# Optimization experiments

Measured on AMD Instinct MI355X. Metric: run time of the kernel, lower is better.

Reference implementation:

```python
import jax, jax.numpy as jnp
import numpy as np
from jax import lax

SOS_TOKEN = 0
PAD_LEN = 30  # tokenizer.pad_len -> number of greedy decode steps


def _gru_cell(x, h, w_ih, w_hh, b_ih, b_hh):
    # PyTorch GRU cell math. x,h: [B,H]; w_*: [3H,H]; b_*: [3H]
    gi = x @ w_ih.T + b_ih
    gh = h @ w_hh.T + b_hh
    i_r, i_z, i_n = jnp.split(gi, 3, axis=-1)
    h_r, h_z, h_n = jnp.split(gh, 3, axis=-1)
    r = jax.nn.sigmoid(i_r + h_r)
    z = jax.nn.sigmoid(i_z + h_z)
    n = jnp.tanh(i_n + r * h_n)
    return (1.0 - z) * n + z * h


def _sm_encode(sm_hidden, conv_w, conv_b, enc_w, enc_b):
    # sm_hidden: [B, L, C] -> conv over time with C input channels
    x = jnp.transpose(sm_hidden, (0, 2, 1))  # [B, C, L]
    conv = lax.conv_general_dilated(
        x, conv_w, window_strides=(1,), padding='VALID',
        dimension_numbers=('NCH', 'OIH', 'NCH'))  # [B, O, L-k+1]
    conv = jax.nn.relu(conv + conv_b[None, :, None])
    pooled = jnp.max(conv, axis=-1)  # [B, O]
    return jax.nn.relu(pooled @ enc_w.T + enc_b)  # [B, H]


def reference(sm_hidden, embedding, w_ih, w_hh, b_ih, b_hh,
              w_out, b_out, conv_w, conv_b, enc_w, enc_b):
    B = sm_hidden.shape[0]
    h0 = _sm_encode(sm_hidden, conv_w, conv_b, enc_w, enc_b)  # [B, H]

    # The original re-runs the GRU over the whole (append-only) prefix each
    # iteration; since the GRU is deterministic this equals incremental
    # single-step updates, which we do here.
    def step(carry, _):
        h, tok = carry
        emb = embedding[tok]                      # [B, H]
        h_new = _gru_cell(emb, h, w_ih, w_hh, b_ih, b_hh)
        logits = h_new @ w_out.T + b_out          # [B, V]
        tok_new = jnp.argmax(logits, axis=-1)     # greedy topk(1)
        return (h_new, tok_new), (h_new, tok_new)

    tok0 = jnp.full((B,), SOS_TOKEN, dtype=jnp.int32)
    (h_last, _), (hiddens, toks) = lax.scan(step, (h0, tok0), None, length=PAD_LEN)

    decoder_output = jax.nn.log_softmax(h_last @ w_out.T + b_out, axis=1)  # [B, V]
    decoder_hidden = hiddens  # [PAD_LEN, B, H] == rnn_out of final _base_forward
    decoded_indices = jnp.concatenate([tok0[None, :], toks], axis=0)  # [PAD_LEN+1, B]
    return decoder_output, decoder_hidden, decoded_indices


def setup_inputs() -> dict:
    key = jax.random.key(0)
    ks = jax.random.split(key, 12)
    B, L, C = 512, 120, 128
    H, V, O, K = 1024, 512, 32, 10
    s = 1.0 / np.sqrt(H)
    return {
        'sm_hidden': jax.random.normal(ks[0], (B, L, C), jnp.float32),
        'embedding': jax.random.normal(ks[1], (V, H), jnp.float32),
        'w_ih': jax.random.uniform(ks[2], (3 * H, H), jnp.float32, -s, s),
        'w_hh': jax.random.uniform(ks[3], (3 * H, H), jnp.float32, -s, s),
        'b_ih': jax.random.uniform(ks[4], (3 * H,), jnp.float32, -s, s),
        'b_hh': jax.random.uniform(ks[5], (3 * H,), jnp.float32, -s, s),
        'w_out': jax.random.uniform(ks[6], (V, H), jnp.float32, -s, s),
        'b_out': jax.random.uniform(ks[7], (V,), jnp.float32, -s, s),
        'conv_w': jax.random.normal(ks[8], (O, C, K), jnp.float32) * 0.05,
        'conv_b': jax.random.normal(ks[9], (O,), jnp.float32) * 0.05,
        'enc_w': jax.random.uniform(ks[10], (H, O), jnp.float32, -s, s),
        'enc_b': jax.random.uniform(ks[11], (H,), jnp.float32, -s, s),
    }
```

## Files before the change

### kernel.cpp

```cpp
#include <hip/hip_runtime.h>
#include <hip/hip_bf16.h>
#include <math.h>

#define Bsz 512
#define Hd 1024
#define Vd 512
#define Cc 128
#define Ll 120
#define Kk 10
#define Oo 32
#define NSTEP 30

typedef __attribute__((ext_vector_type(8))) short bf16x8;
typedef __attribute__((ext_vector_type(4))) float f32x4;
typedef unsigned short ushort;
typedef unsigned long long u64;

static __device__ __forceinline__ float sigm(float x) { return 1.f / (1.f + expf(-x)); }
static __device__ __forceinline__ ushort f2bf(float x) {
    __hip_bfloat16 h = __float2bfloat16(x);
    return *(ushort*)&h;
}
static __device__ __forceinline__ float bf2f(ushort u) {
    __hip_bfloat16 h; *(ushort*)&h = u;
    return __bfloat162float(h);
}
static __device__ __forceinline__ unsigned monofy(float f) {
    unsigned u = __float_as_uint(f);
    return (u & 0x80000000u) ? ~u : (u | 0x80000000u);
}

__global__ void k_split(const float* __restrict__ in, ushort* __restrict__ hi,
                        ushort* __restrict__ lo, int n) {
    int i = blockIdx.x * 256 + threadIdx.x;
    if (i < n) {
        float v = in[i];
        ushort h = f2bf(v);
        hi[i] = h;
        lo[i] = f2bf(v - bf2f(h));
    }
}

__global__ void k_pack(const float* __restrict__ W, ushort* __restrict__ hi,
                       ushort* __restrict__ lo, int total) {
    int idx = blockIdx.x * 256 + threadIdx.x;
    if (idx >= total) return;
    int jj = idx & 7, l = (idx >> 3) & 63, c = (idx >> 9) & 31, nf = idx >> 14;
    int n = nf * 16 + (l & 15);
    int k = c * 32 + ((l >> 4) << 3) + jj;
    float v = W[(size_t)n * 1024 + k];
    ushort h = f2bf(v);
    hi[idx] = h;
    lo[idx] = f2bf(v - bf2f(h));
}

__global__ void k_packconv(const float* __restrict__ cw, ushort* __restrict__ hi,
                           ushort* __restrict__ lo) {
    int idx = blockIdx.x * 256 + threadIdx.x;
    if (idx >= 2 * 40 * 64 * 8) return;
    int jj = idx & 7, l = (idx >> 3) & 63, ch = (idx >> 9) % 40, nf = idx / (40 * 512);
    int o = nf * 16 + (l & 15);
    int k = ch * 32 + ((l >> 4) << 3) + jj;
    int kc = k >> 7, c = k & 127;
    float v = cw[(o * Cc + c) * Kk + kc];
    ushort h = f2bf(v);
    hi[idx] = h;
    lo[idx] = f2bf(v - bf2f(h));
}

__global__ __launch_bounds__(256) void k_convmfma(const ushort* __restrict__ xH,
                                                  const ushort* __restrict__ xL,
                                                  const ushort* __restrict__ wH,
                                                  const ushort* __restrict__ wL,
                                                  const float* __restrict__ cb,
                                                  const float* __restrict__ ew,
                                                  const float* __restrict__ eb,
                                                  float* __restrict__ h0,
                                                  ushort* __restrict__ ApHi,
                                                  ushort* __restrict__ ApLo) {
    __shared__ float sred[4][2][16];
    __shared__ float ps[Oo];
    int tid = threadIdx.x, wid = tid >> 6, l = tid & 63;

    for (int b2 = 0; b2 < 2; ++b2) {
        int b = blockIdx.x * 2 + b2;
        f32x4 acc[2][2];
#pragma unroll
        for (int i = 0; i < 2; ++i)
#pragma unroll
            for (int j = 0; j < 2; ++j) acc[i][j] = (f32x4)0.f;

        bf16x8 aH0[2], aL0[2], bH0[2], bL0[2];
        bf16x8 aH1[2], aL1[2], bH1[2], bL1[2];

#define CLD(AH, AL, BH, BL, ch)                                                        \
    {                                                                                  \
        _Pragma("unroll") for (int tf2 = 0; tf2 < 2; ++tf2) {                          \
            int aoff = ((b * 120 + (wid * 2 + tf2) * 16 + (l & 15) + ((ch) >> 2)) * 128 \
                        + ((ch) & 3) * 32 + ((l >> 4) << 3));                          \
            AH[tf2] = *(const bf16x8*)(xH + aoff);                                     \
            AL[tf2] = *(const bf16x8*)(xL + aoff);                                     \
        }                                                                              \
        _Pragma("unroll") for (int nf = 0; nf < 2; ++nf) {                             \
            int boff = ((nf * 40 + (ch)) * 64 + l) * 8;                                \
            BH[nf] = *(const bf16x8*)(wH + boff);                                      \
            BL[nf] = *(const bf16x8*)(wL + boff);                                      \
        }                                                                              \
    }
#define CST(AH, AL, BH, BL)                                                            \
    {                                                                                  \
        _Pragma("unroll") for (int tf2 = 0; tf2 < 2; ++tf2)                            \
            _Pragma("unroll") for (int nf = 0; nf < 2; ++nf) {                         \
                acc[tf2][nf] = __builtin_amdgcn_mfma_f32_16x16x32_bf16(                \
                    AH[tf2], BH[nf], acc[tf2][nf], 0, 0, 0);                           \
                acc[tf2][nf] = __builtin_amdgcn_mfma_f32_16x16x32_bf16(                \
                    AH[tf2], BL[nf], acc[tf2][nf], 0, 0, 0);                           \
                acc[tf2][nf] = __builtin_amdgcn_mfma_f32_16x16x32_bf16(                \
                    AL[tf2], BH[nf], acc[tf2][nf], 0, 0, 0);                           \
            }                                                                          \
    }

        CLD(aH0, aL0, bH0, bL0, 0)
#pragma unroll
        for (int ch = 0; ch < 40; ch += 2) {
            CLD(aH1, aL1, bH1, bL1, ch + 1)
            CST(aH0, aL0, bH0, bL0)
            if (ch + 2 < 40) CLD(aH0, aL0, bH0, bL0, ch + 2)
            CST(aH1, aL1, bH1, bL1)
        }
#undef CLD
#undef CST

        float mx[2] = {-1e38f, -1e38f};
#pragma unroll
        for (int tf2 = 0; tf2 < 2; ++tf2) {
            int tb = (wid * 2 + tf2) * 16 + ((l >> 4) << 2);
#pragma unroll
            for (int q = 0; q < 4; ++q) {
                if (tb + q <= 110) {
                    mx[0] = fmaxf(mx[0], acc[tf2][0][q]);
                    mx[1] = fmaxf(mx[1], acc[tf2][1][q]);
                }
            }
        }
#pragma unroll
        for (int s = 16; s < 64; s <<= 1) {
            mx[0] = fmaxf(mx[0], __shfl_xor(mx[0], s));
            mx[1] = fmaxf(mx[1], __shfl_xor(mx[1], s));
        }
        if (l < 16) {
            sred[wid][0][l] = mx[0];
            sred[wid][1][l] = mx[1];
        }
        __syncthreads();
        if (tid < Oo) {
            float m = sred[0][tid >> 4][tid & 15];
#pragma unroll
            for (int w = 1; w < 4; ++w) m = fmaxf(m, sred[w][tid >> 4][tid & 15]);
            ps[tid] = fmaxf(m + cb[tid], 0.f);
        }
        __syncthreads();
        for (int j = tid; j < Hd; j += 256) {
            float a = eb[j];
            const float4* e4 = (const float4*)(ew + (size_t)j * Oo);
#pragma unroll
            for (int c4 = 0; c4 < 8; ++c4) {
                float4 w = e4[c4];
                a += ps[c4 * 4 + 0] * w.x + ps[c4 * 4 + 1] * w.y +
                     ps[c4 * 4 + 2] * w.z + ps[c4 * 4 + 3] * w.w;
            }
            a = fmaxf(a, 0.f);
            h0[(size_t)b * Hd + j] = a;
            ushort hb = f2bf(a);
            ushort lb = f2bf(a - bf2f(hb));
            int c = j >> 5, sub = (j >> 3) & 3, jj = j & 7, mf = b >> 4;
            int lane_r = (b & 15) + (sub << 4);
            int flat = ((mf * 32 + c) * 64 + lane_r) * 8 + jj;
            ApHi[flat] = hb;
            ApLo[flat] = lb;
        }
        __syncthreads();
    }
}

template <int EPI>
__global__ __launch_bounds__(512, 4) void k_rnn(const ushort* __restrict__ Ah,
                                                const ushort* __restrict__ Al,
                                                const ushort* __restrict__ Bh,
                                                const ushort* __restrict__ Bl,
                                                const float* __restrict__ bias,
                                                float* __restrict__ outF,
                                                const float* __restrict__ gi_all,
                                                const u64* __restrict__ pkRd,
                                                u64* __restrict__ pkWr,
                                                float* __restrict__ outIdxRow,
                                                const float* __restrict__ hOld,
                                                ushort* __restrict__ ApHi,
                                                ushort* __restrict__ ApLo) {
    __shared__ ushort Bs[2][24][512];
    int id = blockIdx.x;
    int xcd = id & 7, r = id >> 3;
    int jt = xcd * 4 + (r & 3);
    int mt = r >> 2;
    int tid = threadIdx.x, wid = tid >> 6, l = tid & 63;
    int wm = wid >> 1, wj = wid & 1;
    int mf = mt * 4 + wm;
    int jf = jt * 2 + wj;
    int jcol = jf * 16 + (l & 15);

    float giR[4][3], hR[4];
    int bR[4], tkR[4];
    if constexpr (EPI == 1) {
#pragma unroll
        for (int q = 0; q < 4; ++q) {
            bR[q] = mf * 16 + ((l >> 4) << 2) + q;
            u64 pk = pkRd[bR[q]];
            tkR[q] = 511 - (int)(unsigned)(pk & 0xFFFFFFFFu);
            const float* gi = gi_all + (size_t)tkR[q] * 3072;
            giR[q][0] = gi[jcol];
            giR[q][1] = gi[1024 + jcol];
            giR[q][2] = gi[2048 + jcol];
            hR[q] = hOld[(size_t)bR[q] * 1024 + jcol];
        }
        if (jt == 0 && wj == 0 && (l & 15) == 0) {
#pragma unroll
            for (int q = 0; q < 4; ++q) {
                pkWr[bR[q]] = 0ULL;
                if (outIdxRow) outIdxRow[bR[q]] = (float)tkR[q];
            }
        }
    }

    f32x4 acc[3];
#pragma unroll
    for (int g = 0; g < 3; ++g) acc[g] = (f32x4)0.f;

    bf16x8 stg[3], aH0[2], aL0[2], aH1[2], aL1[2];

#define STG_LD(it)                                                                     \
    {                                                                                  \
        _Pragma("unroll") for (int k = 0; k < 3; ++k) {                                \
            int u = wid + 8 * k;                                                       \
            int hl = u & 1, wjb = (u >> 1) & 1, g = (u >> 2) % 3, cu = u / 12;         \
            const ushort* sp = hl ? Bl : Bh;                                           \
            stg[k] = *(const bf16x8*)(sp +                                             \
                (size_t)(((g * 64 + jt * 2 + wjb) * 32 + (it) * 2 + cu) * 64 + l) * 8);\
        }                                                                              \
    }
#define STG_WR(buf)                                                                    \
    {                                                                                  \
        _Pragma("unroll") for (int k = 0; k < 3; ++k)                                  \
            *(bf16x8*)&Bs[buf][wid + 8 * k][l * 8] = stg[k];                           \
    }
#define A_LD(DH, DL, it)                                                               \
    {                                                                                  \
        _Pragma("unroll") for (int cc = 0; cc < 2; ++cc) {                             \
            DH[cc] = *(const bf16x8*)(Ah + (size_t)((mf * 32 + (it) * 2 + cc) * 64 + l) * 8); \
            DL[cc] = *(const bf16x8*)(Al + (size_t)((mf * 32 + (it) * 2 + cc) * 64 + l) * 8); \
        }                                                                              \
    }
#define CMP(buf, AH, AL)                                                               \
    {                                                                                  \
        _Pragma("unroll") for (int cc = 0; cc < 2; ++cc)                               \
            _Pragma("unroll") for (int g = 0; g < 3; ++g) {                            \
                bf16x8 bhh = *(const bf16x8*)&Bs[buf][cc * 12 + g * 4 + wj * 2 + 0][l * 8]; \
                bf16x8 bll = *(const bf16x8*)&Bs[buf][cc * 12 + g * 4 + wj * 2 + 1][l * 8]; \
                acc[g] = __builtin_amdgcn_mfma_f32_16x16x32_bf16(AH[cc], bhh, acc[g], 0, 0, 0); \
                acc[g] = __builtin_amdgcn_mfma_f32_16x16x32_bf16(AH[cc], bll, acc[g], 0, 0, 0); \
                acc[g] = __builtin_amdgcn_mfma_f32_16x16x32_bf16(AL[cc], bhh, acc[g], 0, 0, 0); \
            }                                                                          \
    }

    STG_LD(0)
    STG_WR(0)
    STG_LD(1)
    A_LD(aH0, aL0, 0)
    __syncthreads();
#pragma unroll
    for (int it = 0; it < 16; ++it) {
        int buf = it & 1;
        if (it < 15) STG_WR(buf ^ 1)
        if (it < 14) STG_LD(it + 2)
        if (it & 1) {
            if (it < 15) A_LD(aH0, aL0, it + 1)
            CMP(buf, aH1, aL1)
        } else {
            if (it < 15) A_LD(aH1, aL1, it + 1)
            CMP(buf, aH0, aL0)
        }
        __syncthreads();
    }
#undef STG_LD
#undef STG_WR
#undef A_LD
#undef CMP

    if constexpr (EPI == 0) {
#pragma unroll
        for (int q = 0; q < 4; ++q) {
            int b = mf * 16 + ((l >> 4) << 2) + q;
#pragma unroll
            for (int g = 0; g < 3; ++g)
                outF[(size_t)b * 3072 + g * 1024 + jcol] =
                    acc[g][q] + bias[g * 1024 + jcol];
        }
    } else {
        float bj0 = bias[jcol], bj1 = bias[1024 + jcol], bj2 = bias[2048 + jcol];
        int c = jcol >> 5, sub = (jcol >> 3) & 3, jj = jcol & 7;
#pragma unroll
        for (int q = 0; q < 4; ++q) {
            int b = bR[q];
            float rr = sigm(giR[q][0] + acc[0][q] + bj0);
            float zz = sigm(giR[q][1] + acc[1][q] + bj1);
            float nn = tanhf(giR[q][2] + rr * (acc[2][q] + bj2));
            float hv = (1.f - zz) * nn + zz * hR[q];
            outF[(size_t)b * 1024 + jcol] = hv;
            ushort hb = f2bf(hv);
            ushort lb = f2bf(hv - bf2f(hb));
            int lane_r = (b & 15) + (sub << 4);
            int flat = ((mf * 32 + c) * 64 + lane_r) * 8 + jj;
            ApHi[flat] = hb;
            ApLo[flat] = lb;
        }
    }
}

__global__ __launch_bounds__(256) void k_lgt(const ushort* __restrict__ Ah,
                                             const ushort* __restrict__ Al,
                                             const ushort* __restrict__ Bh,
                                             const ushort* __restrict__ Bl,
                                             const float* __restrict__ bias,
                                             float* __restrict__ outF,
                                             u64* __restrict__ pkOut) {
    int p = blockIdx.x * 4 + (threadIdx.x >> 6);
    int l = threadIdx.x & 63;
    int mf = p >> 5, vf = p & 31;
    size_t ab = (size_t)(mf * 32) * 512 + l * 8;
    size_t bb = (size_t)(vf * 32) * 512 + l * 8;
    f32x4 acc = (f32x4)0.f;
    bf16x8 a0h, a0l, b0h, b0l, a1h, a1l, b1h, b1l;

#define LD1(AH, AL, BH, BL, c)                                                         \
    {                                                                                  \
        AH = *(const bf16x8*)(Ah + ab + (size_t)(c) * 512);                            \
        AL = *(const bf16x8*)(Al + ab + (size_t)(c) * 512);                            \
        BH = *(const bf16x8*)(Bh + bb + (size_t)(c) * 512);                            \
        BL = *(const bf16x8*)(Bl + bb + (size_t)(c) * 512);                            \
    }
#define ST1(AH, AL, BH, BL)                                                            \
    {                                                                                  \
        acc = __builtin_amdgcn_mfma_f32_16x16x32_bf16(AH, BH, acc, 0, 0, 0);           \
        acc = __builtin_amdgcn_mfma_f32_16x16x32_bf16(AH, BL, acc, 0, 0, 0);           \
        acc = __builtin_amdgcn_mfma_f32_16x16x32_bf16(AL, BH, acc, 0, 0, 0);           \
    }

    LD1(a0h, a0l, b0h, b0l, 0)
#pragma unroll
    for (int c = 0; c < 32; c += 2) {
        LD1(a1h, a1l, b1h, b1l, c + 1)
        ST1(a0h, a0l, b0h, b0l)
        if (c + 2 < 32) LD1(a0h, a0l, b0h, b0l, c + 2)
        ST1(a1h, a1l, b1h, b1l)
    }
#undef LD1
#undef ST1

    int v = vf * 16 + (l & 15);
    float bv = bias[v];
    float lg[4];
    unsigned vmq[4];
#pragma unroll
    for (int q = 0; q < 4; ++q) {
        int b = mf * 16 + ((l >> 4) << 2) + q;
        lg[q] = acc[q] + bv;
        outF[(size_t)b * Vd + v] = lg[q];
        vmq[q] = 511u - (unsigned)v;
    }
#pragma unroll
    for (int off = 1; off < 16; off <<= 1) {
#pragma unroll
        for (int q = 0; q < 4; ++q) {
            float og = __shfl_xor(lg[q], off);
            unsigned ov = __shfl_xor(vmq[q], off);
            if (og > lg[q] || (og == lg[q] && ov > vmq[q])) { lg[q] = og; vmq[q] = ov; }
        }
    }
    if ((l & 15) == 0) {
#pragma unroll
        for (int q = 0; q < 4; ++q) {
            int b = mf * 16 + ((l >> 4) << 2) + q;
            u64 pk = ((u64)monofy(lg[q]) << 32) | (u64)vmq[q];
            atomicMax(&pkOut[b], pk);
        }
    }
}

__global__ __launch_bounds__(64) void k_fin(const float* __restrict__ logits,
                                            const u64* __restrict__ pk,
                                            float* __restrict__ out_lsm,
                                            float* __restrict__ outIdxRow) {
    int b = blockIdx.x, l = threadIdx.x;
    const float* row = logits + (size_t)b * Vd;
    float bv = -3.4e38f;
#pragma unroll
    for (int s = 0; s < 8; ++s) bv = fmaxf(bv, row[s * 64 + l]);
#pragma unroll
    for (int off = 1; off < 64; off <<= 1) bv = fmaxf(bv, __shfl_xor(bv, off));
    float sum = 0.f;
#pragma unroll
    for (int s = 0; s < 8; ++s) sum += expf(row[s * 64 + l] - bv);
#pragma unroll
    for (int off = 1; off < 64; off <<= 1) sum += __shfl_xor(sum, off);
    float lse = logf(sum) + bv;
#pragma unroll
    for (int s = 0; s < 8; ++s) {
        int v = s * 64 + l;
        out_lsm[(size_t)b * Vd + v] = row[v] - lse;
    }
    if (l == 0)
        outIdxRow[b] = (float)(511 - (int)(unsigned)(pk[b] & 0xFFFFFFFFu));
}

__global__ void k_init(u64* __restrict__ P0, float* __restrict__ out_idx0) {
    int i = blockIdx.x * 64 + threadIdx.x;
    if (i < Bsz) {
        P0[i] = (1ULL << 32) | 511ULL;
        out_idx0[i] = 0.f;
    }
}

extern "C" void kernel_launch(void* const* d_in, const int* in_sizes, int n_in,
                              void* d_out, int out_size, void* d_ws, size_t ws_size,
                              hipStream_t stream) {
    const float* sm    = (const float*)d_in[0];
    const float* emb   = (const float*)d_in[1];
    const float* w_ih  = (const float*)d_in[2];
    const float* w_hh  = (const float*)d_in[3];
    const float* b_ih  = (const float*)d_in[4];
    const float* b_hh  = (const float*)d_in[5];
    const float* w_out = (const float*)d_in[6];
    const float* b_out = (const float*)d_in[7];
    const float* cw    = (const float*)d_in[8];
    const float* cb    = (const float*)d_in[9];
    const float* ew    = (const float*)d_in[10];
    const float* eb    = (const float*)d_in[11];

    float* out0 = (float*)d_out;
    float* out1 = out0 + (size_t)Bsz * Vd;
    float* out2 = out1 + (size_t)NSTEP * Bsz * Hd;

    const int SMN = Bsz * Ll * Cc;
    char* wsp = (char*)d_ws;
    float*  f_gi  = (float*)wsp;  wsp += sizeof(float) * Bsz * 3072;
    float*  f_h0  = (float*)wsp;  wsp += sizeof(float) * Bsz * Hd;
    float*  f_log = (float*)wsp;  wsp += sizeof(float) * Bsz * Vd;
    u64*    Ppk0  = (u64*)wsp;    wsp += sizeof(u64) * Bsz;
    u64*    Ppk1  = (u64*)wsp;    wsp += sizeof(u64) * Bsz;
    ushort* ApHi0 = (ushort*)wsp; wsp += sizeof(ushort) * Bsz * Hd;
    ushort* ApLo0 = (ushort*)wsp; wsp += sizeof(ushort) * Bsz * Hd;
    ushort* ApHi1 = (ushort*)wsp; wsp += sizeof(ushort) * Bsz * Hd;
    ushort* ApLo1 = (ushort*)wsp; wsp += sizeof(ushort) * Bsz * Hd;
    ushort* embH  = (ushort*)wsp; wsp += sizeof(ushort) * Vd * Hd;
    ushort* embL  = (ushort*)wsp; wsp += sizeof(ushort) * Vd * Hd;
    ushort* wihH  = (ushort*)wsp; wsp += sizeof(ushort) * 3072 * Hd;
    ushort* wihL  = (ushort*)wsp; wsp += sizeof(ushort) * 3072 * Hd;
    ushort* whhH  = (ushort*)wsp; wsp += sizeof(ushort) * 3072 * Hd;
    ushort* whhL  = (ushort*)wsp; wsp += sizeof(ushort) * 3072 * Hd;
    ushort* woutH = (ushort*)wsp; wsp += sizeof(ushort) * Vd * Hd;
    ushort* woutL = (ushort*)wsp; wsp += sizeof(ushort) * Vd * Hd;
    ushort* smH   = (ushort*)wsp; wsp += sizeof(ushort) * (SMN + 32 * Cc);
    ushort* smL   = (ushort*)wsp; wsp += sizeof(ushort) * (SMN + 32 * Cc);
    ushort* cwBH  = (ushort*)wsp; wsp += sizeof(ushort) * 2 * 40 * 64 * 8;
    ushort* cwBL  = (ushort*)wsp; wsp += sizeof(ushort) * 2 * 40 * 64 * 8;

    k_split<<<SMN / 256, 256, 0, stream>>>(sm, smH, smL, SMN);
    k_packconv<<<160, 256, 0, stream>>>(cw, cwBH, cwBL);
    k_pack<<<(3072 * 1024) / 256, 256, 0, stream>>>(w_ih, wihH, wihL, 3072 * 1024);
    k_pack<<<(3072 * 1024) / 256, 256, 0, stream>>>(w_hh, whhH, whhL, 3072 * 1024);
    k_pack<<<(512 * 1024) / 256, 256, 0, stream>>>(w_out, woutH, woutL, 512 * 1024);
    k_pack<<<(512 * 1024) / 256, 256, 0, stream>>>(emb, embH, embL, 512 * 1024);
    k_convmfma<<<256, 256, 0, stream>>>(smH, smL, cwBH, cwBL, cb, ew, eb,
                                        f_h0, ApHi0, ApLo0);
    k_rnn<0><<<256, 512, 0, stream>>>(embH, embL, wihH, wihL, b_ih, f_gi,
                                      nullptr, nullptr, nullptr, nullptr, nullptr,
                                      nullptr, nullptr);
    k_init<<<8, 64, 0, stream>>>(Ppk0, out2);

    ushort* aH[2] = {ApHi0, ApHi1};
    ushort* aL[2] = {ApLo0, ApLo1};
    u64* P[2] = {Ppk0, Ppk1};
    for (int t = 0; t < NSTEP; ++t) {
        int cur = t & 1, nxt = cur ^ 1;
        const float* hOld = (t == 0) ? f_h0 : (out1 + (size_t)(t - 1) * Bsz * Hd);
        k_rnn<1><<<256, 512, 0, stream>>>(
            aH[cur], aL[cur], whhH, whhL, b_hh, out1 + (size_t)t * Bsz * Hd,
            f_gi, P[t & 1], P[(t + 1) & 1],
            (t >= 1) ? (out2 + (size_t)t * Bsz) : nullptr,
            hOld, aH[nxt], aL[nxt]);
        k_lgt<<<256, 256, 0, stream>>>(aH[nxt], aL[nxt], woutH, woutL, b_out,
                                       f_log, P[(t + 1) & 1]);
    }
    k_fin<<<Bsz, 64, 0, stream>>>(f_log, P[NSTEP & 1], out0,
                                  out2 + (size_t)NSTEP * Bsz);
}
```

Measured before the change: 926.6 us.

## Fuse input split into conv, retile GI, recurrent, and logit GEMM kernels

```diff
diff --git a/kernel.cpp b/kernel.cpp
--- a/kernel.cpp
+++ b/kernel.cpp
@@ -28,17 +28,6 @@
 static __device__ __forceinline__ unsigned monofy(float f) {
     unsigned u = __float_as_uint(f);
     return (u & 0x80000000u) ? ~u : (u | 0x80000000u);
-}
-
-__global__ void k_split(const float* __restrict__ in, ushort* __restrict__ hi,
-                        ushort* __restrict__ lo, int n) {
-    int i = blockIdx.x * 256 + threadIdx.x;
-    if (i < n) {
-        float v = in[i];
-        ushort h = f2bf(v);
-        hi[i] = h;
-        lo[i] = f2bf(v - bf2f(h));
-    }
 }
 
 __global__ void k_pack(const float* __restrict__ W, ushort* __restrict__ hi,
@@ -68,8 +57,7 @@
     lo[idx] = f2bf(v - bf2f(h));
 }
 
-__global__ __launch_bounds__(256) void k_convmfma(const ushort* __restrict__ xH,
-                                                  const ushort* __restrict__ xL,
+__global__ __launch_bounds__(256) void k_convmfma(const float* __restrict__ sm,
                                                   const ushort* __restrict__ wH,
                                                   const ushort* __restrict__ wL,
                                                   const float* __restrict__ cb,
@@ -78,28 +66,48 @@
                                                   float* __restrict__ h0,
                                                   ushort* __restrict__ ApHi,
                                                   ushort* __restrict__ ApLo) {
+    __shared__ ushort hiS[137 * 128];
+    __shared__ ushort loS[137 * 128];
     __shared__ float sred[4][2][16];
     __shared__ float ps[Oo];
-    int tid = threadIdx.x, wid = tid >> 6, l = tid & 63;
-
-    for (int b2 = 0; b2 < 2; ++b2) {
-        int b = blockIdx.x * 2 + b2;
-        f32x4 acc[2][2];
-#pragma unroll
-        for (int i = 0; i < 2; ++i)
-#pragma unroll
-            for (int j = 0; j < 2; ++j) acc[i][j] = (f32x4)0.f;
-
-        bf16x8 aH0[2], aL0[2], bH0[2], bL0[2];
-        bf16x8 aH1[2], aL1[2], bH1[2], bL1[2];
+    int b = blockIdx.x, tid = threadIdx.x, wid = tid >> 6, l = tid & 63;
+
+    const float* smb = sm + (size_t)b * (Ll * Cc);
+    for (int i = tid; i < 1920; i += 256) {
+        int row = i >> 4, col0 = (i & 15) * 8;
+        float4 fa = *(const float4*)(smb + row * Cc + col0);
+        float4 fb = *(const float4*)(smb + row * Cc + col0 + 4);
+        float vv[8] = {fa.x, fa.y, fa.z, fa.w, fb.x, fb.y, fb.z, fb.w};
+        ushort h8[8], l8[8];
+#pragma unroll
+        for (int q = 0; q < 8; ++q) {
+            ushort h = f2bf(vv[q]);
+            h8[q] = h;
+            l8[q] = f2bf(vv[q] - bf2f(h));
+        }
+        int o = ((row << 8) + (col0 << 1)) ^ ((row & 7) << 4);
+        *(bf16x8*)((char*)hiS + o) = *(bf16x8*)h8;
+        *(bf16x8*)((char*)loS + o) = *(bf16x8*)l8;
+    }
+    __syncthreads();
+
+    f32x4 acc[2][2];
+#pragma unroll
+    for (int i = 0; i < 2; ++i)
+#pragma unroll
+        for (int j = 0; j < 2; ++j) acc[i][j] = (f32x4)0.f;
+
+    bf16x8 aH0[2], aL0[2], bH0[2], bL0[2];
+    bf16x8 aH1[2], aL1[2], bH1[2], bL1[2];
 
 #define CLD(AH, AL, BH, BL, ch)                                                        \
     {                                                                                  \
         _Pragma("unroll") for (int tf2 = 0; tf2 < 2; ++tf2) {                          \
-            int aoff = ((b * 120 + (wid * 2 + tf2) * 16 + (l & 15) + ((ch) >> 2)) * 128 \
-                        + ((ch) & 3) * 32 + ((l >> 4) << 3));                          \
-            AH[tf2] = *(const bf16x8*)(xH + aoff);                                     \
-            AL[tf2] = *(const bf16x8*)(xL + aoff);                                     \
+            int row = (wid * 2 + tf2) * 16 + (l & 15) + ((ch) >> 2);                   \
+            int o = ((row << 8) + ((((ch) & 3) * 32 + ((l >> 4) << 3)) << 1))          \
+                    ^ ((row & 7) << 4);                                                \
+            AH[tf2] = *(const bf16x8*)((const char*)hiS + o);                          \
+            AL[tf2] = *(const bf16x8*)((const char*)loS + o);                          \
         }                                                                              \
         _Pragma("unroll") for (int nf = 0; nf < 2; ++nf) {                             \
             int boff = ((nf * 40 + (ch)) * 64 + l) * 8;                                \
@@ -120,84 +128,74 @@
             }                                                                          \
     }
 
-        CLD(aH0, aL0, bH0, bL0, 0)
-#pragma unroll
-        for (int ch = 0; ch < 40; ch += 2) {
-            CLD(aH1, aL1, bH1, bL1, ch + 1)
-            CST(aH0, aL0, bH0, bL0)
-            if (ch + 2 < 40) CLD(aH0, aL0, bH0, bL0, ch + 2)
-            CST(aH1, aL1, bH1, bL1)
-        }
+    CLD(aH0, aL0, bH0, bL0, 0)
+#pragma unroll
+    for (int ch = 0; ch < 40; ch += 2) {
+        CLD(aH1, aL1, bH1, bL1, ch + 1)
+        CST(aH0, aL0, bH0, bL0)
+        if (ch + 2 < 40) CLD(aH0, aL0, bH0, bL0, ch + 2)
+        CST(aH1, aL1, bH1, bL1)
+    }
 #undef CLD
 #undef CST
 
-        float mx[2] = {-1e38f, -1e38f};
-#pragma unroll
-        for (int tf2 = 0; tf2 < 2; ++tf2) {
-            int tb = (wid * 2 + tf2) * 16 + ((l >> 4) << 2);
-#pragma unroll
-            for (int q = 0; q < 4; ++q) {
-                if (tb + q <= 110) {
-                    mx[0] = fmaxf(mx[0], acc[tf2][0][q]);
-                    mx[1] = fmaxf(mx[1], acc[tf2][1][q]);
-                }
+    float mx[2] = {-1e38f, -1e38f};
+#pragma unroll
+    for (int tf2 = 0; tf2 < 2; ++tf2) {
+        int tb = (wid * 2 + tf2) * 16 + ((l >> 4) << 2);
+#pragma unroll
+        for (int q = 0; q < 4; ++q) {
+            if (tb + q <= 110) {
+                mx[0] = fmaxf(mx[0], acc[tf2][0][q]);
+                mx[1] = fmaxf(mx[1], acc[tf2][1][q]);
             }
         }
-#pragma unroll
-        for (int s = 16; s < 64; s <<= 1) {
-            mx[0] = fmaxf(mx[0], __shfl_xor(mx[0], s));
-            mx[1] = fmaxf(mx[1], __shfl_xor(mx[1], s));
-        }
-        if (l < 16) {
-            sred[wid][0][l] = mx[0];
-            sred[wid][1][l] = mx[1];
-        }
-        __syncthreads();
-        if (tid < Oo) {
-            float m = sred[0][tid >> 4][tid & 15];
-#pragma unroll
-            for (int w = 1; w < 4; ++w) m = fmaxf(m, sred[w][tid >> 4][tid & 15]);
-            ps[tid] = fmaxf(m + cb[tid], 0.f);
-        }
-        __syncthreads();
-        for (int j = tid; j < Hd; j += 256) {
-            float a = eb[j];
-            const float4* e4 = (const float4*)(ew + (size_t)j * Oo);
-#pragma unroll
-            for (int c4 = 0; c4 < 8; ++c4) {
-                float4 w = e4[c4];
-                a += ps[c4 * 4 + 0] * w.x + ps[c4 * 4 + 1] * w.y +
-                     ps[c4 * 4 + 2] * w.z + ps[c4 * 4 + 3] * w.w;
-            }
-            a = fmaxf(a, 0.f);
-            h0[(size_t)b * Hd + j] = a;
-            ushort hb = f2bf(a);
-            ushort lb = f2bf(a - bf2f(hb));
-            int c = j >> 5, sub = (j >> 3) & 3, jj = j & 7, mf = b >> 4;
-            int lane_r = (b & 15) + (sub << 4);
-            int flat = ((mf * 32 + c) * 64 + lane_r) * 8 + jj;
-            ApHi[flat] = hb;
-            ApLo[flat] = lb;
-        }
-        __syncthreads();
-    }
-}
-
-template <int EPI>
-__global__ __launch_bounds__(512, 4) void k_rnn(const ushort* __restrict__ Ah,
-                                                const ushort* __restrict__ Al,
-                                                const ushort* __restrict__ Bh,
-                                                const ushort* __restrict__ Bl,
-                                                const float* __restrict__ bias,
-                                                float* __restrict__ outF,
-                                                const float* __restrict__ gi_all,
-                                                const u64* __restrict__ pkRd,
-                                                u64* __restrict__ pkWr,
-                                                float* __restrict__ outIdxRow,
-                                                const float* __restrict__ hOld,
-                                                ushort* __restrict__ ApHi,
-                                                ushort* __restrict__ ApLo) {
-    __shared__ ushort Bs[2][24][512];
+    }
+#pragma unroll
+    for (int s = 16; s < 64; s <<= 1) {
+        mx[0] = fmaxf(mx[0], __shfl_xor(mx[0], s));
+        mx[1] = fmaxf(mx[1], __shfl_xor(mx[1], s));
+    }
+    if (l < 16) {
+        sred[wid][0][l] = mx[0];
+        sred[wid][1][l] = mx[1];
+    }
+    __syncthreads();
+    if (tid < Oo) {
+        float m = sred[0][tid >> 4][tid & 15];
+#pragma unroll
+        for (int w = 1; w < 4; ++w) m = fmaxf(m, sred[w][tid >> 4][tid & 15]);
+        ps[tid] = fmaxf(m + cb[tid], 0.f);
+    }
+    __syncthreads();
+    for (int j = tid; j < Hd; j += 256) {
+        float a = eb[j];
+        const float4* e4 = (const float4*)(ew + (size_t)j * Oo);
+#pragma unroll
+        for (int c4 = 0; c4 < 8; ++c4) {
+            float4 w = e4[c4];
+            a += ps[c4 * 4 + 0] * w.x + ps[c4 * 4 + 1] * w.y +
+                 ps[c4 * 4 + 2] * w.z + ps[c4 * 4 + 3] * w.w;
+        }
+        a = fmaxf(a, 0.f);
+        h0[(size_t)b * Hd + j] = a;
+        ushort hb = f2bf(a);
+        ushort lb = f2bf(a - bf2f(hb));
+        int c = j >> 5, sub = (j >> 3) & 3, jj = j & 7, amf = b >> 4;
+        int lane_r = (b & 15) + (sub << 4);
+        int flat = ((amf * 32 + c) * 64 + lane_r) * 8 + jj;
+        ApHi[flat] = hb;
+        ApLo[flat] = lb;
+    }
+}
+
+__global__ __launch_bounds__(512, 2) void k_gi(const ushort* __restrict__ Ah,
+                                               const ushort* __restrict__ Al,
+                                               const ushort* __restrict__ Bh,
+                                               const ushort* __restrict__ Bl,
+                                               const float* __restrict__ bias,
+                                               float* __restrict__ outF) {
+    __shared__ ushort Bs[2][48][512];
     int id = blockIdx.x;
     int xcd = id & 7, r = id >> 3;
     int jt = xcd * 4 + (r & 3);
@@ -208,60 +206,37 @@
     int jf = jt * 2 + wj;
     int jcol = jf * 16 + (l & 15);
 
-    float giR[4][3], hR[4];
-    int bR[4], tkR[4];
-    if constexpr (EPI == 1) {
-#pragma unroll
-        for (int q = 0; q < 4; ++q) {
-            bR[q] = mf * 16 + ((l >> 4) << 2) + q;
-            u64 pk = pkRd[bR[q]];
-            tkR[q] = 511 - (int)(unsigned)(pk & 0xFFFFFFFFu);
-            const float* gi = gi_all + (size_t)tkR[q] * 3072;
-            giR[q][0] = gi[jcol];
-            giR[q][1] = gi[1024 + jcol];
-            giR[q][2] = gi[2048 + jcol];
-            hR[q] = hOld[(size_t)bR[q] * 1024 + jcol];
-        }
-        if (jt == 0 && wj == 0 && (l & 15) == 0) {
-#pragma unroll
-            for (int q = 0; q < 4; ++q) {
-                pkWr[bR[q]] = 0ULL;
-                if (outIdxRow) outIdxRow[bR[q]] = (float)tkR[q];
-            }
-        }
-    }
-
     f32x4 acc[3];
 #pragma unroll
     for (int g = 0; g < 3; ++g) acc[g] = (f32x4)0.f;
 
-    bf16x8 stg[3], aH0[2], aL0[2], aH1[2], aL1[2];
+    bf16x8 stg[6], aH0[4], aL0[4], aH1[4], aL1[4];
 
 #define STG_LD(it)                                                                     \
     {                                                                                  \
-        _Pragma("unroll") for (int k = 0; k < 3; ++k) {                                \
+        _Pragma("unroll") for (int k = 0; k < 6; ++k) {                                \
             int u = wid + 8 * k;                                                       \
             int hl = u & 1, wjb = (u >> 1) & 1, g = (u >> 2) % 3, cu = u / 12;         \
             const ushort* sp = hl ? Bl : Bh;                                           \
             stg[k] = *(const bf16x8*)(sp +                                             \
-                (size_t)(((g * 64 + jt * 2 + wjb) * 32 + (it) * 2 + cu) * 64 + l) * 8);\
+                (size_t)(((g * 64 + jt * 2 + wjb) * 32 + (it) * 4 + cu) * 64 + l) * 8);\
         }                                                                              \
     }
 #define STG_WR(buf)                                                                    \
     {                                                                                  \
-        _Pragma("unroll") for (int k = 0; k < 3; ++k)                                  \
+        _Pragma("unroll") for (int k = 0; k < 6; ++k)                                  \
             *(bf16x8*)&Bs[buf][wid + 8 * k][l * 8] = stg[k];                           \
     }
 #define A_LD(DH, DL, it)                                                               \
     {                                                                                  \
-        _Pragma("unroll") for (int cc = 0; cc < 2; ++cc) {                             \
-            DH[cc] = *(const bf16x8*)(Ah + (size_t)((mf * 32 + (it) * 2 + cc) * 64 + l) * 8); \
-            DL[cc] = *(const bf16x8*)(Al + (size_t)((mf * 32 + (it) * 2 + cc) * 64 + l) * 8); \
+        _Pragma("unroll") for (int cc = 0; cc < 4; ++cc) {                             \
+            DH[cc] = *(const bf16x8*)(Ah + (size_t)((mf * 32 + (it) * 4 + cc) * 64 + l) * 8); \
+            DL[cc] = *(const bf16x8*)(Al + (size_t)((mf * 32 + (it) * 4 + cc) * 64 + l) * 8); \
         }                                                                              \
     }
 #define CMP(buf, AH, AL)                                                               \
     {                                                                                  \
-        _Pragma("unroll") for (int cc = 0; cc < 2; ++cc)                               \
+        _Pragma("unroll") for (int cc = 0; cc < 4; ++cc)                               \
             _Pragma("unroll") for (int g = 0; g < 3; ++g) {                            \
                 bf16x8 bhh = *(const bf16x8*)&Bs[buf][cc * 12 + g * 4 + wj * 2 + 0][l * 8]; \
                 bf16x8 bll = *(const bf16x8*)&Bs[buf][cc * 12 + g * 4 + wj * 2 + 1][l * 8]; \
@@ -277,15 +252,15 @@
     A_LD(aH0, aL0, 0)
     __syncthreads();
 #pragma unroll
-    for (int it = 0; it < 16; ++it) {
+    for (int it = 0; it < 8; ++it) {
         int buf = it & 1;
-        if (it < 15) STG_WR(buf ^ 1)
-        if (it < 14) STG_LD(it + 2)
+        if (it < 7) STG_WR(buf ^ 1)
+        if (it < 6) STG_LD(it + 2)
         if (it & 1) {
-            if (it < 15) A_LD(aH0, aL0, it + 1)
+            if (it < 7) A_LD(aH0, aL0, it + 1)
             CMP(buf, aH1, aL1)
         } else {
-            if (it < 15) A_LD(aH1, aL1, it + 1)
+            if (it < 7) A_LD(aH1, aL1, it + 1)
             CMP(buf, aH0, aL0)
         }
         __syncthreads();
@@ -295,32 +270,131 @@
 #undef A_LD
 #undef CMP
 
-    if constexpr (EPI == 0) {
+#pragma unroll
+    for (int q = 0; q < 4; ++q) {
+        int b = mf * 16 + ((l >> 4) << 2) + q;
+#pragma unroll
+        for (int g = 0; g < 3; ++g)
+            outF[(size_t)b * 3072 + g * 1024 + jcol] = acc[g][q] + bias[g * 1024 + jcol];
+    }
+}
+
+__global__ __launch_bounds__(256) void k_rnn2(const ushort* __restrict__ Ah,
+                                              const ushort* __restrict__ Al,
+                                              const ushort* __restrict__ Bh,
+                                              const ushort* __restrict__ Bl,
+                                              const float* __restrict__ bias,
+                                              float* __restrict__ outF,
+                                              const float* __restrict__ gi_all,
+                                              const u64* __restrict__ pkRd,
+                                              u64* __restrict__ pkWr,
+                                              float* __restrict__ outIdxRow,
+                                              const float* __restrict__ hOld,
+                                              ushort* __restrict__ ApHi,
+                                              ushort* __restrict__ ApLo) {
+    __shared__ ushort Bs[2][12][512];
+    int id = blockIdx.x;
+    int xcd = id & 7, r = id >> 3;
+    int jf = xcd * 8 + (r & 7);
+    int mt = r >> 3;
+    int tid = threadIdx.x, w = tid >> 6, l = tid & 63;
+    int jcol = jf * 16 + (l & 15);
+
+    f32x4 acc[2][3];
+#pragma unroll
+    for (int m = 0; m < 2; ++m)
+#pragma unroll
+        for (int g = 0; g < 3; ++g) acc[m][g] = (f32x4)0.f;
+
+    bf16x8 stg[3], ah[2][2], al[2][2];
+
+#define RSTG_LD(it)                                                                    \
+    {                                                                                  \
+        _Pragma("unroll") for (int k = 0; k < 3; ++k) {                                \
+            int s = tid + 256 * k;                                                     \
+            int il = s & 63, u = s >> 6;                                               \
+            int hl = u & 1, g = (u >> 1) % 3, cu = u / 6;                              \
+            const ushort* sp = hl ? Bl : Bh;                                           \
+            stg[k] = *(const bf16x8*)(sp +                                             \
+                (size_t)(((g * 64 + jf) * 32 + (it) * 2 + cu) * 64 + il) * 8);         \
+        }                                                                              \
+    }
+#define RSTG_WR(buf)                                                                   \
+    {                                                                                  \
+        _Pragma("unroll") for (int k = 0; k < 3; ++k) {                                \
+            int s = tid + 256 * k;                                                     \
+            int il = s & 63, u = s >> 6;                                               \
+            *(bf16x8*)&Bs[buf][u][il * 8] = stg[k];                                    \
+        }                                                                              \
+    }
+#define RA_LD(it)                                                                      \
+    {                                                                                  \
+        _Pragma("unroll") for (int cc = 0; cc < 2; ++cc)                               \
+            _Pragma("unroll") for (int m = 0; m < 2; ++m) {                            \
+                size_t off = (size_t)(((mt * 8 + w * 2 + m) * 32 + (it) * 2 + cc) * 64 \
+                                      + l) * 8;                                        \
+                ah[cc][m] = *(const bf16x8*)(Ah + off);                                \
+                al[cc][m] = *(const bf16x8*)(Al + off);                                \
+            }                                                                          \
+    }
+#define RCMP(buf)                                                                      \
+    {                                                                                  \
+        _Pragma("unroll") for (int cc = 0; cc < 2; ++cc)                               \
+            _Pragma("unroll") for (int g = 0; g < 3; ++g) {                            \
+                bf16x8 bh = *(const bf16x8*)&Bs[buf][cc * 6 + g * 2 + 0][l * 8];       \
+                bf16x8 bl = *(const bf16x8*)&Bs[buf][cc * 6 + g * 2 + 1][l * 8];       \
+                _Pragma("unroll") for (int m = 0; m < 2; ++m) {                        \
+                    acc[m][g] = __builtin_amdgcn_mfma_f32_16x16x32_bf16(ah[cc][m], bh, acc[m][g], 0, 0, 0); \
+                    acc[m][g] = __builtin_amdgcn_mfma_f32_16x16x32_bf16(ah[cc][m], bl, acc[m][g], 0, 0, 0); \
+                    acc[m][g] = __builtin_amdgcn_mfma_f32_16x16x32_bf16(al[cc][m], bh, acc[m][g], 0, 0, 0); \
+                }                                                                      \
+            }                                                                          \
+    }
+
+    RSTG_LD(0)
+    RSTG_WR(0)
+    RSTG_LD(1)
+    __syncthreads();
+#pragma unroll
+    for (int it = 0; it < 16; ++it) {
+        int buf = it & 1;
+        if (it < 15) RSTG_WR(buf ^ 1)
+        if (it < 14) RSTG_LD(it + 2)
+        RA_LD(it)
+        RCMP(buf)
+        __syncthreads();
+    }
+#undef RSTG_LD
+#undef RSTG_WR
+#undef RA_LD
+#undef RCMP
+
+    float bj0 = bias[jcol], bj1 = bias[1024 + jcol], bj2 = bias[2048 + jcol];
+    int c = jcol >> 5, sub = (jcol >> 3) & 3, jj = jcol & 7;
+#pragma unroll
+    for (int m = 0; m < 2; ++m) {
+        int mf = mt * 8 + w * 2 + m;
 #pragma unroll
         for (int q = 0; q < 4; ++q) {
             int b = mf * 16 + ((l >> 4) << 2) + q;
-#pragma unroll
-            for (int g = 0; g < 3; ++g)
-                outF[(size_t)b * 3072 + g * 1024 + jcol] =
-                    acc[g][q] + bias[g * 1024 + jcol];
-        }
-    } else {
-        float bj0 = bias[jcol], bj1 = bias[1024 + jcol], bj2 = bias[2048 + jcol];
-        int c = jcol >> 5, sub = (jcol >> 3) & 3, jj = jcol & 7;
-#pragma unroll
-        for (int q = 0; q < 4; ++q) {
-            int b = bR[q];
-            float rr = sigm(giR[q][0] + acc[0][q] + bj0);
-            float zz = sigm(giR[q][1] + acc[1][q] + bj1);
-            float nn = tanhf(giR[q][2] + rr * (acc[2][q] + bj2));
-            float hv = (1.f - zz) * nn + zz * hR[q];
+            u64 pk = pkRd[b];
+            int tk = 511 - (int)(unsigned)(pk & 0xFFFFFFFFu);
+            const float* gi = gi_all + (size_t)tk * 3072;
+            float rr = sigm(gi[jcol] + acc[m][0][q] + bj0);
+            float zz = sigm(gi[1024 + jcol] + acc[m][1][q] + bj1);
+            float nn = tanhf(gi[2048 + jcol] + rr * (acc[m][2][q] + bj2));
+            float hv = (1.f - zz) * nn + zz * hOld[(size_t)b * 1024 + jcol];
             outF[(size_t)b * 1024 + jcol] = hv;
             ushort hb = f2bf(hv);
             ushort lb = f2bf(hv - bf2f(hb));
             int lane_r = (b & 15) + (sub << 4);
-            int flat = ((mf * 32 + c) * 64 + lane_r) * 8 + jj;
+            int flat = (((b >> 4) * 32 + c) * 64 + lane_r) * 8 + jj;
             ApHi[flat] = hb;
             ApLo[flat] = lb;
+            if (jf == 0 && (l & 15) == 0) {
+                pkWr[b] = 0ULL;
+                if (outIdxRow) outIdxRow[b] = (float)tk;
+            }
         }
     }
 }
@@ -332,38 +406,61 @@
                                              const float* __restrict__ bias,
                                              float* __restrict__ outF,
                                              u64* __restrict__ pkOut) {
-    int p = blockIdx.x * 4 + (threadIdx.x >> 6);
-    int l = threadIdx.x & 63;
-    int mf = p >> 5, vf = p & 31;
-    size_t ab = (size_t)(mf * 32) * 512 + l * 8;
-    size_t bb = (size_t)(vf * 32) * 512 + l * 8;
+    __shared__ ushort Bs[2][8][512];
+    int id = blockIdx.x;
+    int xcd = id & 7, r = id >> 3;
+    int vf = xcd * 4 + (r & 3);
+    int mg = r >> 2;
+    int tid = threadIdx.x, w = tid >> 6, l = tid & 63;
+    int mf = mg * 4 + w;
+
     f32x4 acc = (f32x4)0.f;
-    bf16x8 a0h, a0l, b0h, b0l, a1h, a1l, b1h, b1l;
-
-#define LD1(AH, AL, BH, BL, c)                                                         \
-    {                                                                                  \
-        AH = *(const bf16x8*)(Ah + ab + (size_t)(c) * 512);                            \
-        AL = *(const bf16x8*)(Al + ab + (size_t)(c) * 512);                            \
-        BH = *(const bf16x8*)(Bh + bb + (size_t)(c) * 512);                            \
-        BL = *(const bf16x8*)(Bl + bb + (size_t)(c) * 512);                            \
-    }
-#define ST1(AH, AL, BH, BL)                                                            \
-    {                                                                                  \
-        acc = __builtin_amdgcn_mfma_f32_16x16x32_bf16(AH, BH, acc, 0, 0, 0);           \
-        acc = __builtin_amdgcn_mfma_f32_16x16x32_bf16(AH, BL, acc, 0, 0, 0);           \
-        acc = __builtin_amdgcn_mfma_f32_16x16x32_bf16(AL, BH, acc, 0, 0, 0);           \
-    }
-
-    LD1(a0h, a0l, b0h, b0l, 0)
-#pragma unroll
-    for (int c = 0; c < 32; c += 2) {
-        LD1(a1h, a1l, b1h, b1l, c + 1)
-        ST1(a0h, a0l, b0h, b0l)
-        if (c + 2 < 32) LD1(a0h, a0l, b0h, b0l, c + 2)
-        ST1(a1h, a1l, b1h, b1l)
-    }
-#undef LD1
-#undef ST1
+    bf16x8 stg[2], ah, al;
+
+#define LSTG_LD(it)                                                                    \
+    {                                                                                  \
+        _Pragma("unroll") for (int k = 0; k < 2; ++k) {                                \
+            int s = tid + 256 * k;                                                     \
+            int il = s & 63, u = s >> 6;                                               \
+            int hl = u & 1, cu = u >> 1;                                               \
+            const ushort* sp = hl ? Bl : Bh;                                           \
+            stg[k] = *(const bf16x8*)(sp +                                             \
+                (size_t)((vf * 32 + (it) * 4 + cu) * 64 + il) * 8);                    \
+        }                                                                              \
+    }
+#define LSTG_WR(buf)                                                                   \
+    {                                                                                  \
+        _Pragma("unroll") for (int k = 0; k < 2; ++k) {                                \
+            int s = tid + 256 * k;                                                     \
+            int il = s & 63, u = s >> 6;                                               \
+            *(bf16x8*)&Bs[buf][u][il * 8] = stg[k];                                    \
+        }                                                                              \
+    }
+
+    LSTG_LD(0)
+    LSTG_WR(0)
+    LSTG_LD(1)
+    __syncthreads();
+#pragma unroll
+    for (int it = 0; it < 8; ++it) {
+        int buf = it & 1;
+        if (it < 7) LSTG_WR(buf ^ 1)
+        if (it < 6) LSTG_LD(it + 2)
+#pragma unroll
+        for (int cu = 0; cu < 4; ++cu) {
+            size_t aoff = (size_t)((mf * 32 + it * 4 + cu) * 64 + l) * 8;
+            ah = *(const bf16x8*)(Ah + aoff);
+            al = *(const bf16x8*)(Al + aoff);
+            bf16x8 bh = *(const bf16x8*)&Bs[buf][cu * 2 + 0][l * 8];
+            bf16x8 bl = *(const bf16x8*)&Bs[buf][cu * 2 + 1][l * 8];
+            acc = __builtin_amdgcn_mfma_f32_16x16x32_bf16(ah, bh, acc, 0, 0, 0);
+            acc = __builtin_amdgcn_mfma_f32_16x16x32_bf16(ah, bl, acc, 0, 0, 0);
+            acc = __builtin_amdgcn_mfma_f32_16x16x32_bf16(al, bh, acc, 0, 0, 0);
+        }
+        __syncthreads();
+    }
+#undef LSTG_LD
+#undef LSTG_WR
 
     int v = vf * 16 + (l & 15);
     float bv = bias[v];
@@ -449,7 +546,6 @@
     float* out1 = out0 + (size_t)Bsz * Vd;
     float* out2 = out1 + (size_t)NSTEP * Bsz * Hd;
 
-    const int SMN = Bsz * Ll * Cc;
     char* wsp = (char*)d_ws;
     float*  f_gi  = (float*)wsp;  wsp += sizeof(float) * Bsz * 3072;
     float*  f_h0  = (float*)wsp;  wsp += sizeof(float) * Bsz * Hd;
@@ -468,22 +564,17 @@
     ushort* whhL  = (ushort*)wsp; wsp += sizeof(ushort) * 3072 * Hd;
     ushort* woutH = (ushort*)wsp; wsp += sizeof(ushort) * Vd * Hd;
     ushort* woutL = (ushort*)wsp; wsp += sizeof(ushort) * Vd * Hd;
-    ushort* smH   = (ushort*)wsp; wsp += sizeof(ushort) * (SMN + 32 * Cc);
-    ushort* smL   = (ushort*)wsp; wsp += sizeof(ushort) * (SMN + 32 * Cc);
     ushort* cwBH  = (ushort*)wsp; wsp += sizeof(ushort) * 2 * 40 * 64 * 8;
     ushort* cwBL  = (ushort*)wsp; wsp += sizeof(ushort) * 2 * 40 * 64 * 8;
 
-    k_split<<<SMN / 256, 256, 0, stream>>>(sm, smH, smL, SMN);
     k_packconv<<<160, 256, 0, stream>>>(cw, cwBH, cwBL);
     k_pack<<<(3072 * 1024) / 256, 256, 0, stream>>>(w_ih, wihH, wihL, 3072 * 1024);
     k_pack<<<(3072 * 1024) / 256, 256, 0, stream>>>(w_hh, whhH, whhL, 3072 * 1024);
     k_pack<<<(512 * 1024) / 256, 256, 0, stream>>>(w_out, woutH, woutL, 512 * 1024);
     k_pack<<<(512 * 1024) / 256, 256, 0, stream>>>(emb, embH, embL, 512 * 1024);
-    k_convmfma<<<256, 256, 0, stream>>>(smH, smL, cwBH, cwBL, cb, ew, eb,
+    k_convmfma<<<Bsz, 256, 0, stream>>>(sm, cwBH, cwBL, cb, ew, eb,
                                         f_h0, ApHi0, ApLo0);
-    k_rnn<0><<<256, 512, 0, stream>>>(embH, embL, wihH, wihL, b_ih, f_gi,
-                                      nullptr, nullptr, nullptr, nullptr, nullptr,
-                                      nullptr, nullptr);
+    k_gi<<<256, 512, 0, stream>>>(embH, embL, wihH, wihL, b_ih, f_gi);
     k_init<<<8, 64, 0, stream>>>(Ppk0, out2);
 
     ushort* aH[2] = {ApHi0, ApHi1};
@@ -492,7 +583,7 @@
     for (int t = 0; t < NSTEP; ++t) {
         int cur = t & 1, nxt = cur ^ 1;
         const float* hOld = (t == 0) ? f_h0 : (out1 + (size_t)(t - 1) * Bsz * Hd);
-        k_rnn<1><<<256, 512, 0, stream>>>(
+        k_rnn2<<<256, 256, 0, stream>>>(
             aH[cur], aL[cur], whhH, whhL, b_hh, out1 + (size_t)t * Bsz * Hd,
             f_gi, P[t & 1], P[(t + 1) & 1],
             (t >= 1) ? (out2 + (size_t)t * Bsz) : nullptr,
```

After: 1.229 ms. +32.6%, slower.
